# Kernel tuning notes

Hardware: AMD Instinct MI355X
Metric: run time of the kernel (lower is better)

Reference implementation:

```python
import jax, jax.numpy as jnp
import numpy as np

N_NODES = 50000
N_EDGES = 800000
D_IN = 128
HIDDEN = [128, 128]
D_OUT = 64


def setup_inputs() -> dict:
    key = jax.random.key(0)
    ks = jax.random.split(key, 12)
    x = jax.random.normal(ks[0], (N_NODES, D_IN), dtype=jnp.float32)
    edge_index = jax.random.randint(ks[1], (2, N_EDGES), 0, N_NODES, dtype=jnp.int64)
    # SAGEConv params: lin_l acts on aggregated neighbors (has bias), lin_r on root
    def lin(k, fan_in, fan_out):
        s = 1.0 / np.sqrt(fan_in)
        return jax.random.uniform(k, (fan_in, fan_out), jnp.float32, -s, s)
    dims = [D_IN] + HIDDEN
    inp = {"x": x, "edge_index": edge_index}
    for i in range(len(HIDDEN)):
        inp[f"Wl{i}"] = lin(ks[2 + 3 * i], dims[i], dims[i + 1])
        inp[f"Wr{i}"] = lin(ks[3 + 3 * i], dims[i], dims[i + 1])
        inp[f"b{i}"] = jnp.zeros((dims[i + 1],), jnp.float32)
    inp["Wfc"] = lin(ks[10], HIDDEN[-1], D_OUT)
    inp["bfc"] = jnp.zeros((D_OUT,), jnp.float32)
    return inp


def _sage_conv(x, src, dst, n, Wl, Wr, b, deg_inv):
    # mean-aggregate source features into destination nodes
    agg = jax.ops.segment_sum(x[src], dst, num_segments=n) * deg_inv[:, None]
    return agg @ Wl + x @ Wr + b


def reference(x, edge_index, Wl0, Wr0, b0, Wl1, Wr1, b1, Wfc, bfc):
    src, dst = edge_index[0], edge_index[1]
    n = x.shape[0]
    deg = jax.ops.segment_sum(jnp.ones((src.shape[0],), x.dtype), dst, num_segments=n)
    deg_inv = 1.0 / jnp.maximum(deg, 1.0)
    h = jax.nn.relu(_sage_conv(x, src, dst, n, Wl0, Wr0, b0, deg_inv))
    # dropout p=0 / eval mode -> identity
    h = jax.nn.relu(_sage_conv(h, src, dst, n, Wl1, Wr1, b1, deg_inv))
    return h @ Wfc + bfc
```

## Files before the change

kernel.cpp:

```cpp
#include <hip/hip_runtime.h>
#include <hip/hip_bf16.h>

#define NN 50000
#define NE 800000
#define D 128
#define DOUT 64
#define PAD 64
#define BSH 8
#define NBUCK 196
#define CAP 4608
#define CHUNK 4096

typedef __attribute__((ext_vector_type(8))) short short8;
typedef __attribute__((ext_vector_type(4))) float float4v;


__device__ inline unsigned short f2bf(float f) {
    union { float f; unsigned int i; } c; c.f = f;
    unsigned int u = c.i;
    return (unsigned short)((u + 0x7fffu + ((u >> 16) & 1u)) >> 16);
}
__device__ inline float bflo(unsigned int u) {
    union { unsigned int i; float f; } c; c.i = u << 16; return c.f;
}
__device__ inline float bfhi(unsigned int u) {
    union { unsigned int i; float f; } c; c.i = u & 0xffff0000u; return c.f;
}


__global__ void cast_f32_bf16(const float* __restrict__ in, unsigned short* __restrict__ outb, int n8) {
    int i = blockIdx.x * 256 + threadIdx.x;
    if (i >= n8) return;
    const float4* p = (const float4*)in + (size_t)i * 2;
    float4 a = p[0], b = p[1];
    unsigned int w0 = f2bf(a.x) | ((unsigned int)f2bf(a.y) << 16);
    unsigned int w1 = f2bf(a.z) | ((unsigned int)f2bf(a.w) << 16);
    unsigned int w2 = f2bf(b.x) | ((unsigned int)f2bf(b.y) << 16);
    unsigned int w3 = f2bf(b.z) | ((unsigned int)f2bf(b.w) << 16);
    *(uint4*)(outb + (size_t)i * 8) = make_uint4(w0, w1, w2, w3);
}


struct PackArgs {
    const float* W[5];
    unsigned short* P[5];
    int* gcur;
};

__global__ void pack_all(PackArgs args) {
    if (blockIdx.x == 36) {
        if (threadIdx.x < NBUCK) args.gcur[threadIdx.x] = 0;
        return;
    }
    int idx = blockIdx.x * 256 + threadIdx.x;
    if (idx >= 4 * 2048 + 1024) return;
    const float* W;
    unsigned short* P;
    int COLS, local;
    if (idx < 4 * 2048) {
        int wsel = idx >> 11;
        W = args.W[wsel]; P = args.P[wsel]; COLS = 128; local = idx & 2047;
    } else {
        W = args.W[4]; P = args.P[4]; COLS = 64; local = idx - 4 * 2048;
    }
    int CT = COLS >> 4;
    int lane = local & 63;
    int fi = local >> 6;
    int ct = fi % CT;
    int kstep = fi / CT;
    int krow = kstep * 32 + (lane >> 4) * 8;
    int col = ct * 16 + (lane & 15);
    unsigned short v[8];
#pragma unroll
    for (int j = 0; j < 8; ++j) v[j] = f2bf(W[(size_t)(krow + j) * COLS + col]);
    unsigned int w0 = v[0] | ((unsigned int)v[1] << 16);
    unsigned int w1 = v[2] | ((unsigned int)v[3] << 16);
    unsigned int w2 = v[4] | ((unsigned int)v[5] << 16);
    unsigned int w3 = v[6] | ((unsigned int)v[7] << 16);
    *(uint4*)(P + (size_t)local * 8) = make_uint4(w0, w1, w2, w3);
}


__global__ void bin_edges(const int* __restrict__ src, const int* __restrict__ dst,
                          int* __restrict__ gcur, unsigned int* __restrict__ binned, int e) {
    __shared__ int cnt[NBUCK];
    __shared__ int sh[256];
    __shared__ int baseg[NBUCK];
    __shared__ int lcur[NBUCK];
    __shared__ unsigned int buf[CHUNK];
    int tid = threadIdx.x;
    int base = blockIdx.x * CHUNK;
    for (int b = tid; b < NBUCK; b += 256) cnt[b] = 0;
    __syncthreads();
    unsigned int rec[16];
#pragma unroll
    for (int i = 0; i < 16; ++i) {
        int ei = base + i * 256 + tid;
        rec[i] = 0xffffffffu;
        if (ei < e) {
            unsigned int d = (unsigned int)dst[ei];
            unsigned int s = (unsigned int)src[ei];
            rec[i] = (d << 16) | s;
            atomicAdd(&cnt[d >> BSH], 1);
        }
    }
    __syncthreads();
    int v = (tid < NBUCK) ? cnt[tid] : 0;
    sh[tid] = v;
    __syncthreads();
    for (int off = 1; off < 256; off <<= 1) {
        int t = (tid >= off) ? sh[tid - off] : 0;
        __syncthreads();
        sh[tid] += t;
        __syncthreads();
    }
    if (tid < NBUCK) {
        baseg[tid] = atomicAdd(&gcur[tid], cnt[tid]);
        lcur[tid] = sh[tid] - cnt[tid];
    }
    __syncthreads();
    int total = sh[255];
#pragma unroll
    for (int i = 0; i < 16; ++i) {
        if (rec[i] != 0xffffffffu) {
            int b = rec[i] >> 24;
            int pos = atomicAdd(&lcur[b], 1);
            buf[pos] = rec[i];
        }
    }
    __syncthreads();
    for (int j = tid; j < total; j += 256) {
        unsigned int r = buf[j];
        int b = r >> 24;
        int gidx = baseg[b] + (j - (sh[b] - cnt[b]));
        if (gidx < CAP) binned[(size_t)b * CAP + gidx] = r;
    }
}


__global__ void scatter_bucket(const unsigned int* __restrict__ binned, const int* __restrict__ gcur,
                               unsigned short* __restrict__ eidx_pad, int* __restrict__ cursor) {
    __shared__ int cur[256];
    int b = blockIdx.x;
    int tid = threadIdx.x;
    cur[tid] = 0;
    __syncthreads();
    int count = gcur[b];
    if (count > CAP) count = CAP;
    const unsigned int* seg = binned + (size_t)b * CAP;
    for (int j = tid; j < count; j += 256) {
        unsigned int r = seg[j];
        int dl = (r >> 16) & 255;
        int slot = atomicAdd(&cur[dl], 1);
        if (slot < PAD)
            eidx_pad[((size_t)((b << BSH) + dl)) * PAD + slot] = (unsigned short)(r & 0xffffu);
    }
    __syncthreads();
    int node = (b << BSH) + tid;
    if (node < NN) cursor[node] = (cur[tid] < PAD) ? cur[tid] : PAD;
}


template <bool FUSEFC>
__global__ __launch_bounds__(256, 4)
void fused_layer(const unsigned short* __restrict__ feat,
                 const int* __restrict__ cursor, const unsigned short* __restrict__ eidx_pad,
                 const unsigned short* __restrict__ Pl, const unsigned short* __restrict__ Pr,
                 const float* __restrict__ bias,
                 const unsigned short* __restrict__ Pfc, const float* __restrict__ bfc,
                 unsigned short* __restrict__ outb, float* __restrict__ outf, int n) {
    __shared__ __align__(16) unsigned short As[64][136];

    int tid = threadIdx.x;
    int row0 = blockIdx.x * 64;

    {
        int g = tid >> 4;
        int l = tid & 15;
#pragma unroll
        for (int nn = 0; nn < 4; ++nn) {
            int r = g * 4 + nn;
            int node = row0 + r;
            float acc[8] = {0.f, 0.f, 0.f, 0.f, 0.f, 0.f, 0.f, 0.f};
            float di = 1.f;
            if (node < n) {
                int deg = cursor[node];
                di = 1.0f / (float)(deg > 1 ? deg : 1);
                const unsigned short* rowp = eidx_pad + (size_t)node * PAD;
                int p = 0;
                for (; p + 7 < deg; p += 8) {
                    uint4 iv = *(const uint4*)(rowp + p);
                    int s0 = iv.x & 0xffff, s1 = iv.x >> 16;
                    int s2 = iv.y & 0xffff, s3 = iv.y >> 16;
                    int s4 = iv.z & 0xffff, s5 = iv.z >> 16;
                    int s6 = iv.w & 0xffff, s7 = iv.w >> 16;
                    uint4 v0 = *(const uint4*)(feat + (size_t)s0 * D + l * 8);
                    uint4 v1 = *(const uint4*)(feat + (size_t)s1 * D + l * 8);
                    uint4 v2 = *(const uint4*)(feat + (size_t)s2 * D + l * 8);
                    uint4 v3 = *(const uint4*)(feat + (size_t)s3 * D + l * 8);
                    uint4 v4 = *(const uint4*)(feat + (size_t)s4 * D + l * 8);
                    uint4 v5 = *(const uint4*)(feat + (size_t)s5 * D + l * 8);
                    uint4 v6 = *(const uint4*)(feat + (size_t)s6 * D + l * 8);
                    uint4 v7 = *(const uint4*)(feat + (size_t)s7 * D + l * 8);
                    acc[0] += ((bflo(v0.x) + bflo(v1.x)) + (bflo(v2.x) + bflo(v3.x)))
                            + ((bflo(v4.x) + bflo(v5.x)) + (bflo(v6.x) + bflo(v7.x)));
                    acc[1] += ((bfhi(v0.x) + bfhi(v1.x)) + (bfhi(v2.x) + bfhi(v3.x)))
                            + ((bfhi(v4.x) + bfhi(v5.x)) + (bfhi(v6.x) + bfhi(v7.x)));
                    acc[2] += ((bflo(v0.y) + bflo(v1.y)) + (bflo(v2.y) + bflo(v3.y)))
                            + ((bflo(v4.y) + bflo(v5.y)) + (bflo(v6.y) + bflo(v7.y)));
                    acc[3] += ((bfhi(v0.y) + bfhi(v1.y)) + (bfhi(v2.y) + bfhi(v3.y)))
                            + ((bfhi(v4.y) + bfhi(v5.y)) + (bfhi(v6.y) + bfhi(v7.y)));
                    acc[4] += ((bflo(v0.z) + bflo(v1.z)) + (bflo(v2.z) + bflo(v3.z)))
                            + ((bflo(v4.z) + bflo(v5.z)) + (bflo(v6.z) + bflo(v7.z)));
                    acc[5] += ((bfhi(v0.z) + bfhi(v1.z)) + (bfhi(v2.z) + bfhi(v3.z)))
                            + ((bfhi(v4.z) + bfhi(v5.z)) + (bfhi(v6.z) + bfhi(v7.z)));
                    acc[6] += ((bflo(v0.w) + bflo(v1.w)) + (bflo(v2.w) + bflo(v3.w)))
                            + ((bflo(v4.w) + bflo(v5.w)) + (bflo(v6.w) + bflo(v7.w)));
                    acc[7] += ((bfhi(v0.w) + bfhi(v1.w)) + (bfhi(v2.w) + bfhi(v3.w)))
                            + ((bfhi(v4.w) + bfhi(v5.w)) + (bfhi(v6.w) + bfhi(v7.w)));
                }
                if (p + 3 < deg) {
                    uint2 iv = *(const uint2*)(rowp + p);
                    int s0 = iv.x & 0xffff, s1 = iv.x >> 16;
                    int s2 = iv.y & 0xffff, s3 = iv.y >> 16;
                    uint4 v0 = *(const uint4*)(feat + (size_t)s0 * D + l * 8);
                    uint4 v1 = *(const uint4*)(feat + (size_t)s1 * D + l * 8);
                    uint4 v2 = *(const uint4*)(feat + (size_t)s2 * D + l * 8);
                    uint4 v3 = *(const uint4*)(feat + (size_t)s3 * D + l * 8);
                    acc[0] += (bflo(v0.x) + bflo(v1.x)) + (bflo(v2.x) + bflo(v3.x));
                    acc[1] += (bfhi(v0.x) + bfhi(v1.x)) + (bfhi(v2.x) + bfhi(v3.x));
                    acc[2] += (bflo(v0.y) + bflo(v1.y)) + (bflo(v2.y) + bflo(v3.y));
                    acc[3] += (bfhi(v0.y) + bfhi(v1.y)) + (bfhi(v2.y) + bfhi(v3.y));
                    acc[4] += (bflo(v0.z) + bflo(v1.z)) + (bflo(v2.z) + bflo(v3.z));
                    acc[5] += (bfhi(v0.z) + bfhi(v1.z)) + (bfhi(v2.z) + bfhi(v3.z));
                    acc[6] += (bflo(v0.w) + bflo(v1.w)) + (bflo(v2.w) + bflo(v3.w));
                    acc[7] += (bfhi(v0.w) + bfhi(v1.w)) + (bfhi(v2.w) + bfhi(v3.w));
                    p += 4;
                }
                for (; p < deg; ++p) {
                    int s = rowp[p];
                    uint4 v0 = *(const uint4*)(feat + (size_t)s * D + l * 8);
                    acc[0] += bflo(v0.x); acc[1] += bfhi(v0.x);
                    acc[2] += bflo(v0.y); acc[3] += bfhi(v0.y);
                    acc[4] += bflo(v0.z); acc[5] += bfhi(v0.z);
                    acc[6] += bflo(v0.w); acc[7] += bfhi(v0.w);
                }
            }
            unsigned int w0 = f2bf(acc[0] * di) | ((unsigned int)f2bf(acc[1] * di) << 16);
            unsigned int w1 = f2bf(acc[2] * di) | ((unsigned int)f2bf(acc[3] * di) << 16);
            unsigned int w2 = f2bf(acc[4] * di) | ((unsigned int)f2bf(acc[5] * di) << 16);
            unsigned int w3 = f2bf(acc[6] * di) | ((unsigned int)f2bf(acc[7] * di) << 16);
            *(uint4*)&As[r][l * 8] = make_uint4(w0, w1, w2, w3);
        }
    }
    __syncthreads();

    int wave = tid >> 6;
    int lane = tid & 63;
    int m16 = lane & 15;
    int quad = lane >> 4;
    int rt0 = (wave & 1) * 32;
    int ctb = (wave >> 1) * 4;

    float4v acc[2][4];
#pragma unroll
    for (int t = 0; t < 2; ++t)
#pragma unroll
        for (int c = 0; c < 4; ++c) acc[t][c] = (float4v){0.f, 0.f, 0.f, 0.f};

#pragma unroll
    for (int ks = 0; ks < 4; ++ks) {
        short8 af[2];
#pragma unroll
        for (int t = 0; t < 2; ++t)
            af[t] = *(const short8*)&As[rt0 + t * 16 + m16][ks * 32 + quad * 8];
#pragma unroll
        for (int c = 0; c < 4; ++c) {
            short8 bf = *(const short8*)(Pl + ((size_t)((ks * 8 + ctb + c) * 64 + lane)) * 8);
#pragma unroll
            for (int t = 0; t < 2; ++t)
                acc[t][c] = __builtin_amdgcn_mfma_f32_16x16x32_bf16(af[t], bf, acc[t][c], 0, 0, 0);
        }
    }
#pragma unroll
    for (int ks = 0; ks < 4; ++ks) {
        short8 xf[2];
#pragma unroll
        for (int t = 0; t < 2; ++t) {
            int row = row0 + rt0 + t * 16 + m16;
            short8 z = {0, 0, 0, 0, 0, 0, 0, 0};
            xf[t] = (row < n) ? *(const short8*)(feat + (size_t)row * D + ks * 32 + quad * 8) : z;
        }
#pragma unroll
        for (int c = 0; c < 4; ++c) {
            short8 bf = *(const short8*)(Pr + ((size_t)((ks * 8 + ctb + c) * 64 + lane)) * 8);
#pragma unroll
            for (int t = 0; t < 2; ++t)
                acc[t][c] = __builtin_amdgcn_mfma_f32_16x16x32_bf16(xf[t], bf, acc[t][c], 0, 0, 0);
        }
    }

    if (!FUSEFC) {
#pragma unroll
        for (int t = 0; t < 2; ++t) {
#pragma unroll
            for (int c = 0; c < 4; ++c) {
                int col = (ctb + c) * 16 + m16;
                float bv = bias[col];
#pragma unroll
                for (int i = 0; i < 4; ++i) {
                    int row = row0 + rt0 + t * 16 + quad * 4 + i;
                    if (row < n)
                        outb[(size_t)row * D + col] = f2bf(fmaxf(acc[t][c][i] + bv, 0.f));
                }
            }
        }
    } else {
        __syncthreads();
#pragma unroll
        for (int t = 0; t < 2; ++t) {
#pragma unroll
            for (int c = 0; c < 4; ++c) {
                int col = (ctb + c) * 16 + m16;
                float bv = bias[col];
#pragma unroll
                for (int i = 0; i < 4; ++i) {
                    int row = rt0 + t * 16 + quad * 4 + i;
                    As[row][col] = f2bf(fmaxf(acc[t][c][i] + bv, 0.f));
                }
            }
        }
        __syncthreads();

        int ctbF = (wave >> 1) * 2;
        float4v acc2[2][2];
#pragma unroll
        for (int t = 0; t < 2; ++t)
#pragma unroll
            for (int c = 0; c < 2; ++c) acc2[t][c] = (float4v){0.f, 0.f, 0.f, 0.f};
#pragma unroll
        for (int ks = 0; ks < 4; ++ks) {
            short8 hf[2];
#pragma unroll
            for (int t = 0; t < 2; ++t)
                hf[t] = *(const short8*)&As[rt0 + t * 16 + m16][ks * 32 + quad * 8];
#pragma unroll
            for (int c = 0; c < 2; ++c) {
                short8 bf = *(const short8*)(Pfc + ((size_t)((ks * 4 + ctbF + c) * 64 + lane)) * 8);
#pragma unroll
                for (int t = 0; t < 2; ++t)
                    acc2[t][c] = __builtin_amdgcn_mfma_f32_16x16x32_bf16(hf[t], bf, acc2[t][c], 0, 0, 0);
            }
        }
#pragma unroll
        for (int t = 0; t < 2; ++t) {
#pragma unroll
            for (int c = 0; c < 2; ++c) {
                int col = (ctbF + c) * 16 + m16;
                float bv = bfc[col];
#pragma unroll
                for (int i = 0; i < 4; ++i) {
                    int row = row0 + rt0 + t * 16 + quad * 4 + i;
                    if (row < n)
                        outf[(size_t)row * DOUT + col] = acc2[t][c][i] + bv;
                }
            }
        }
    }
}


extern "C" void kernel_launch(void* const* d_in, const int* in_sizes, int n_in,
                              void* d_out, int out_size, void* d_ws, size_t ws_size,
                              hipStream_t stream) {
    const float* x   = (const float*)d_in[0];
    const int*   ei  = (const int*)d_in[1];
    const float* Wl0 = (const float*)d_in[2];
    const float* Wr0 = (const float*)d_in[3];
    const float* b0  = (const float*)d_in[4];
    const float* Wl1 = (const float*)d_in[5];
    const float* Wr1 = (const float*)d_in[6];
    const float* b1  = (const float*)d_in[7];
    const float* Wfc = (const float*)d_in[8];
    const float* bfc = (const float*)d_in[9];
    float* out = (float*)d_out;

    const int* src = ei;
    const int* dst = ei + NE;

    char* p = (char*)d_ws;
    auto carve = [&](size_t bytes) {
        char* q = p;
        p += (bytes + 255) & ~(size_t)255;
        return q;
    };
    int*            cursor   = (int*)carve(NN * sizeof(int));
    int*            gcur     = (int*)carve(NBUCK * sizeof(int));
    unsigned int*   binned   = (unsigned int*)carve((size_t)NBUCK * CAP * 4);
    unsigned short* eidx_pad = (unsigned short*)carve((size_t)NN * PAD * 2);
    unsigned short* xb   = (unsigned short*)carve((size_t)NN * D * 2);
    unsigned short* h0b  = (unsigned short*)carve((size_t)NN * D * 2);
    unsigned short* Wl0p = (unsigned short*)carve(D * D * 2);
    unsigned short* Wr0p = (unsigned short*)carve(D * D * 2);
    unsigned short* Wl1p = (unsigned short*)carve(D * D * 2);
    unsigned short* Wr1p = (unsigned short*)carve(D * D * 2);
    unsigned short* Wfcp = (unsigned short*)carve(D * DOUT * 2);

    const int N8 = NN * D / 8;
    cast_f32_bf16<<<(N8 + 255) / 256, 256, 0, stream>>>(x, xb, N8);

    PackArgs pa;
    pa.W[0] = Wl0; pa.W[1] = Wr0; pa.W[2] = Wl1; pa.W[3] = Wr1; pa.W[4] = Wfc;
    pa.P[0] = Wl0p; pa.P[1] = Wr0p; pa.P[2] = Wl1p; pa.P[3] = Wr1p; pa.P[4] = Wfcp;
    pa.gcur = gcur;
    pack_all<<<37, 256, 0, stream>>>(pa);

    const int BINB = (NE + CHUNK - 1) / CHUNK;
    bin_edges<<<BINB, 256, 0, stream>>>(src, dst, gcur, binned, NE);
    scatter_bucket<<<NBUCK, 256, 0, stream>>>(binned, gcur, eidx_pad, cursor);

    const int GB = (NN + 63) / 64;

    fused_layer<false><<<GB, 256, 0, stream>>>(xb, cursor, eidx_pad, Wl0p, Wr0p, b0,
                                               nullptr, nullptr, h0b, nullptr, NN);
    fused_layer<true><<<GB, 256, 0, stream>>>(h0b, cursor, eidx_pad, Wl1p, Wr1p, b1,
                                              Wfcp, bfc, nullptr, out, NN);
}
```

Measured before the change: 199.0 us.

## Double threads per block in fused layers and scatter, halve bin chunk

The fused SAGE layer kernels now launch 512 threads per 64-row tile. Each 16-lane group aggregates 2 nodes instead of 4, and each wave computes one 16-row MFMA strip instead of two, which raises parallelism in the latency-bound gather. scatter_bucket also uses 512 threads, and bin_edges processes 2048-edge chunks, which doubles its block count. The cost is more per-block overhead, twice as many global atomics on the bucket cursors, and weight fragments reloaded by more waves.

```diff
diff --git a/kernel.cpp b/kernel.cpp
--- a/kernel.cpp
+++ b/kernel.cpp
@@ -9,7 +9,7 @@
 #define BSH 8
 #define NBUCK 196
 #define CAP 4608
-#define CHUNK 4096
+#define CHUNK 2048
 
 typedef __attribute__((ext_vector_type(8))) short short8;
 typedef __attribute__((ext_vector_type(4))) float float4v;
@@ -92,9 +92,9 @@
     int base = blockIdx.x * CHUNK;
     for (int b = tid; b < NBUCK; b += 256) cnt[b] = 0;
     __syncthreads();
-    unsigned int rec[16];
-#pragma unroll
-    for (int i = 0; i < 16; ++i) {
+    unsigned int rec[8];
+#pragma unroll
+    for (int i = 0; i < 8; ++i) {
         int ei = base + i * 256 + tid;
         rec[i] = 0xffffffffu;
         if (ei < e) {
@@ -121,7 +121,7 @@
     __syncthreads();
     int total = sh[255];
 #pragma unroll
-    for (int i = 0; i < 16; ++i) {
+    for (int i = 0; i < 8; ++i) {
         if (rec[i] != 0xffffffffu) {
             int b = rec[i] >> 24;
             int pos = atomicAdd(&lcur[b], 1);
@@ -143,12 +143,12 @@
     __shared__ int cur[256];
     int b = blockIdx.x;
     int tid = threadIdx.x;
-    cur[tid] = 0;
+    if (tid < 256) cur[tid] = 0;
     __syncthreads();
     int count = gcur[b];
     if (count > CAP) count = CAP;
     const unsigned int* seg = binned + (size_t)b * CAP;
-    for (int j = tid; j < count; j += 256) {
+    for (int j = tid; j < count; j += 512) {
         unsigned int r = seg[j];
         int dl = (r >> 16) & 255;
         int slot = atomicAdd(&cur[dl], 1);
@@ -156,13 +156,15 @@
             eidx_pad[((size_t)((b << BSH) + dl)) * PAD + slot] = (unsigned short)(r & 0xffffu);
     }
     __syncthreads();
-    int node = (b << BSH) + tid;
-    if (node < NN) cursor[node] = (cur[tid] < PAD) ? cur[tid] : PAD;
+    if (tid < 256) {
+        int node = (b << BSH) + tid;
+        if (node < NN) cursor[node] = (cur[tid] < PAD) ? cur[tid] : PAD;
+    }
 }
 
 
 template <bool FUSEFC>
-__global__ __launch_bounds__(256, 4)
+__global__ __launch_bounds__(512, 8)
 void fused_layer(const unsigned short* __restrict__ feat,
                  const int* __restrict__ cursor, const unsigned short* __restrict__ eidx_pad,
                  const unsigned short* __restrict__ Pl, const unsigned short* __restrict__ Pr,
@@ -178,8 +180,8 @@
         int g = tid >> 4;
         int l = tid & 15;
 #pragma unroll
-        for (int nn = 0; nn < 4; ++nn) {
-            int r = g * 4 + nn;
+        for (int nn = 0; nn < 2; ++nn) {
+            int r = g * 2 + nn;
             int node = row0 + r;
             float acc[8] = {0.f, 0.f, 0.f, 0.f, 0.f, 0.f, 0.f, 0.f};
             float di = 1.f;
@@ -259,111 +261,82 @@
     int lane = tid & 63;
     int m16 = lane & 15;
     int quad = lane >> 4;
-    int rt0 = (wave & 1) * 32;
-    int ctb = (wave >> 1) * 4;
-
-    float4v acc[2][4];
-#pragma unroll
-    for (int t = 0; t < 2; ++t)
-#pragma unroll
-        for (int c = 0; c < 4; ++c) acc[t][c] = (float4v){0.f, 0.f, 0.f, 0.f};
+    int rt0 = (wave & 3) * 16;
+    int ctb = (wave >> 2) * 4;
+
+    float4v acc[4];
+#pragma unroll
+    for (int c = 0; c < 4; ++c) acc[c] = (float4v){0.f, 0.f, 0.f, 0.f};
 
 #pragma unroll
     for (int ks = 0; ks < 4; ++ks) {
-        short8 af[2];
-#pragma unroll
-        for (int t = 0; t < 2; ++t)
-            af[t] = *(const short8*)&As[rt0 + t * 16 + m16][ks * 32 + quad * 8];
+        short8 af = *(const short8*)&As[rt0 + m16][ks * 32 + quad * 8];
 #pragma unroll
         for (int c = 0; c < 4; ++c) {
             short8 bf = *(const short8*)(Pl + ((size_t)((ks * 8 + ctb + c) * 64 + lane)) * 8);
-#pragma unroll
-            for (int t = 0; t < 2; ++t)
-                acc[t][c] = __builtin_amdgcn_mfma_f32_16x16x32_bf16(af[t], bf, acc[t][c], 0, 0, 0);
+            acc[c] = __builtin_amdgcn_mfma_f32_16x16x32_bf16(af, bf, acc[c], 0, 0, 0);
         }
     }
 #pragma unroll
     for (int ks = 0; ks < 4; ++ks) {
-        short8 xf[2];
-#pragma unroll
-        for (int t = 0; t < 2; ++t) {
-            int row = row0 + rt0 + t * 16 + m16;
-            short8 z = {0, 0, 0, 0, 0, 0, 0, 0};
-            xf[t] = (row < n) ? *(const short8*)(feat + (size_t)row * D + ks * 32 + quad * 8) : z;
-        }
+        int row = row0 + rt0 + m16;
+        short8 z = {0, 0, 0, 0, 0, 0, 0, 0};
+        short8 xf = (row < n) ? *(const short8*)(feat + (size_t)row * D + ks * 32 + quad * 8) : z;
 #pragma unroll
         for (int c = 0; c < 4; ++c) {
             short8 bf = *(const short8*)(Pr + ((size_t)((ks * 8 + ctb + c) * 64 + lane)) * 8);
-#pragma unroll
-            for (int t = 0; t < 2; ++t)
-                acc[t][c] = __builtin_amdgcn_mfma_f32_16x16x32_bf16(xf[t], bf, acc[t][c], 0, 0, 0);
+            acc[c] = __builtin_amdgcn_mfma_f32_16x16x32_bf16(xf, bf, acc[c], 0, 0, 0);
         }
     }
 
     if (!FUSEFC) {
 #pragma unroll
-        for (int t = 0; t < 2; ++t) {
-#pragma unroll
-            for (int c = 0; c < 4; ++c) {
-                int col = (ctb + c) * 16 + m16;
-                float bv = bias[col];
-#pragma unroll
-                for (int i = 0; i < 4; ++i) {
-                    int row = row0 + rt0 + t * 16 + quad * 4 + i;
-                    if (row < n)
-                        outb[(size_t)row * D + col] = f2bf(fmaxf(acc[t][c][i] + bv, 0.f));
-                }
+        for (int c = 0; c < 4; ++c) {
+            int col = (ctb + c) * 16 + m16;
+            float bv = bias[col];
+#pragma unroll
+            for (int i = 0; i < 4; ++i) {
+                int row = row0 + rt0 + quad * 4 + i;
+                if (row < n)
+                    outb[(size_t)row * D + col] = f2bf(fmaxf(acc[c][i] + bv, 0.f));
             }
         }
     } else {
         __syncthreads();
 #pragma unroll
-        for (int t = 0; t < 2; ++t) {
-#pragma unroll
-            for (int c = 0; c < 4; ++c) {
-                int col = (ctb + c) * 16 + m16;
-                float bv = bias[col];
-#pragma unroll
-                for (int i = 0; i < 4; ++i) {
-                    int row = rt0 + t * 16 + quad * 4 + i;
-                    As[row][col] = f2bf(fmaxf(acc[t][c][i] + bv, 0.f));
-                }
+        for (int c = 0; c < 4; ++c) {
+            int col = (ctb + c) * 16 + m16;
+            float bv = bias[col];
+#pragma unroll
+            for (int i = 0; i < 4; ++i) {
+                int row = rt0 + quad * 4 + i;
+                As[row][col] = f2bf(fmaxf(acc[c][i] + bv, 0.f));
             }
         }
         __syncthreads();
 
-        int ctbF = (wave >> 1) * 2;
-        float4v acc2[2][2];
-#pragma unroll
-        for (int t = 0; t < 2; ++t)
-#pragma unroll
-            for (int c = 0; c < 2; ++c) acc2[t][c] = (float4v){0.f, 0.f, 0.f, 0.f};
+        int ctbF = (wave >> 2) * 2;
+        float4v acc2[2];
+#pragma unroll
+        for (int c = 0; c < 2; ++c) acc2[c] = (float4v){0.f, 0.f, 0.f, 0.f};
 #pragma unroll
         for (int ks = 0; ks < 4; ++ks) {
-            short8 hf[2];
-#pragma unroll
-            for (int t = 0; t < 2; ++t)
-                hf[t] = *(const short8*)&As[rt0 + t * 16 + m16][ks * 32 + quad * 8];
+            short8 hf = *(const short8*)&As[rt0 + m16][ks * 32 + quad * 8];
 #pragma unroll
             for (int c = 0; c < 2; ++c) {
                 short8 bf = *(const short8*)(Pfc + ((size_t)((ks * 4 + ctbF + c) * 64 + lane)) * 8);
-#pragma unroll
-                for (int t = 0; t < 2; ++t)
-                    acc2[t][c] = __builtin_amdgcn_mfma_f32_16x16x32_bf16(hf[t], bf, acc2[t][c], 0, 0, 0);
+                acc2[c] = __builtin_amdgcn_mfma_f32_16x16x32_bf16(hf, bf, acc2[c], 0, 0, 0);
             }
         }
 #pragma unroll
-        for (int t = 0; t < 2; ++t) {
-#pragma unroll
-            for (int c = 0; c < 2; ++c) {
-                int col = (ctbF + c) * 16 + m16;
-                float bv = bfc[col];
-#pragma unroll
-                for (int i = 0; i < 4; ++i) {
-                    int row = row0 + rt0 + t * 16 + quad * 4 + i;
-                    if (row < n)
-                        outf[(size_t)row * DOUT + col] = acc2[t][c][i] + bv;
-                }
+        for (int c = 0; c < 2; ++c) {
+            int col = (ctbF + c) * 16 + m16;
+            float bv = bfc[col];
+#pragma unroll
+            for (int i = 0; i < 4; ++i) {
+                int row = row0 + rt0 + quad * 4 + i;
+                if (row < n)
+                    outf[(size_t)row * DOUT + col] = acc2[c][i] + bv;
             }
         }
     }
@@ -417,12 +390,12 @@
 
     const int BINB = (NE + CHUNK - 1) / CHUNK;
     bin_edges<<<BINB, 256, 0, stream>>>(src, dst, gcur, binned, NE);
-    scatter_bucket<<<NBUCK, 256, 0, stream>>>(binned, gcur, eidx_pad, cursor);
+    scatter_bucket<<<NBUCK, 512, 0, stream>>>(binned, gcur, eidx_pad, cursor);
 
     const int GB = (NN + 63) / 64;
 
-    fused_layer<false><<<GB, 256, 0, stream>>>(xb, cursor, eidx_pad, Wl0p, Wr0p, b0,
+    fused_layer<false><<<GB, 512, 0, stream>>>(xb, cursor, eidx_pad, Wl0p, Wr0p, b0,
                                                nullptr, nullptr, h0b, nullptr, NN);
-    fused_layer<true><<<GB, 256, 0, stream>>>(h0b, cursor, eidx_pad, Wl1p, Wr1p, b1,
+    fused_layer<true><<<GB, 512, 0, stream>>>(h0b, cursor, eidx_pad, Wl1p, Wr1p, b1,
                                               Wfcp, bfc, nullptr, out, NN);
 }
```

New measurement: 211.4 us. 6.2% more time.
